# Kernel optimization log

Hardware: AMD Instinct MI355X
Metric: run time of the kernel (lower is better)

Reference implementation:

```python
import jax, jax.numpy as jnp
import numpy as np

HIDDEN = 768
FFN = 3072
E = 8
TOP_K = 2


def setup_inputs() -> dict:
    key = jax.random.key(0)
    k_x, k_r, k_w1, k_w2 = jax.random.split(key, 4)
    x = jax.random.normal(k_x, (1, 1024, HIDDEN), dtype=jnp.float32)
    # nn.Linear(hidden, E, bias=False): weight applied as x @ W^T; store as [H, E]
    bound = 1.0 / np.sqrt(HIDDEN)
    router_w = jax.random.uniform(k_r, (HIDDEN, E), minval=-bound, maxval=bound, dtype=jnp.float32)
    w1 = jax.random.normal(k_w1, (E, HIDDEN, FFN), dtype=jnp.float32) * 0.02
    w2 = jax.random.normal(k_w2, (E, FFN, HIDDEN), dtype=jnp.float32) * 0.02
    return {"x": x, "router_w": router_w, "w1": w1, "w2": w2}


def reference(x, router_w, w1, w2):
    B, T, H = x.shape
    xf = x.reshape(-1, H)                                  # [N, H]
    logits = xf @ router_w                                 # [N, E] (eval mode: no noise)
    probs = jax.nn.softmax(logits, axis=-1)
    top_v, top_i = jax.lax.top_k(probs, TOP_K)             # [N, K]
    top_v = top_v / jnp.sum(top_v, axis=-1, keepdims=True)  # renormalize top-k probs
    # Combine top-k weights into a dense per-expert gate; zero gates make the
    # dense per-expert computation mathematically identical to sparse dispatch.
    gates = jnp.sum(jax.nn.one_hot(top_i, E, dtype=xf.dtype) * top_v[..., None], axis=1)  # [N, E]
    h = jax.nn.gelu(jnp.einsum('nh,ehf->enf', xf, w1), approximate=False)  # [E, N, F]
    y = jnp.einsum('enf,efh->enh', h, w2)                  # [E, N, H]
    out = jnp.einsum('ne,enh->nh', gates, y)               # [N, H]
    return out.reshape(B, T, H)
```

## Files before the change

kernel.cpp:

```cpp
#include <hip/hip_runtime.h>
#include <cmath>

#define NTOK 1024
#define HD   768
#define FF   3072
#define NE   8
#define NSLOT (NTOK * 2)
#define BK   64
#define CLD  130

#define NB_ROUTER 256
#define NB_CONV1  2304
#define NB_CONV2  2304
#define NB_FFN1   3072

typedef unsigned short u16;
typedef unsigned int   u32;
typedef __bf16 bf16x8 __attribute__((ext_vector_type(8)));
typedef float  f32x4  __attribute__((ext_vector_type(4)));
typedef u16    u16x8  __attribute__((ext_vector_type(8)));

__device__ __forceinline__ u16 f2bf(float f) {
  union { float f; u32 u; } v; v.f = f;
  u32 r = v.u + 0x7FFFu + ((v.u >> 16) & 1u);
  return (u16)(r >> 16);
}

__device__ __forceinline__ void load16(const void* g, void* l) {
  __builtin_amdgcn_global_load_lds(
      (const __attribute__((address_space(1))) u32*)g,
      (__attribute__((address_space(3))) u32*)l, 16, 0, 0);
}

__device__ __forceinline__ void conv_tile(
    const float* __restrict__ src, u16* __restrict__ dst,
    int K, int N, int k0, int n0, char* smem, int tid, int lane, int wid)
{
  u16* lt = (u16*)smem;
  const int rr = tid >> 4;
  const int cc = (tid & 15) << 2;

  const float* s0 = src + (size_t)(k0 + rr) * N + n0 + cc;
  float4 v[8];
#pragma unroll
  for (int j = 0; j < 8; ++j) v[j] = *(const float4*)(s0 + (size_t)j * 16 * N);
  __builtin_amdgcn_sched_barrier(0);

#pragma unroll
  for (int j = 0; j < 8; ++j) {
    const int k = j * 16 + rr;
    lt[(cc + 0) * CLD + k] = f2bf(v[j].x); lt[(cc + 1) * CLD + k] = f2bf(v[j].y);
    lt[(cc + 2) * CLD + k] = f2bf(v[j].z); lt[(cc + 3) * CLD + k] = f2bf(v[j].w);
  }
  __syncthreads();

  const int l15 = lane & 15;
  const int r4  = lane >> 4;
#pragma unroll
  for (int s = 0; s < 4; ++s) {
    const int r = wid * 16 + s * 4 + r4;
    u16x8 vv;
#pragma unroll
    for (int d = 0; d < 8; ++d) vv[d] = lt[r * CLD + l15 * 8 + d];
    *(u16x8*)(dst + (size_t)(n0 + r) * K + k0 + l15 * 8) = vv;
  }
}

__global__ __launch_bounds__(256, 4) void conv1_router_kernel(
    const float* __restrict__ w1, u16* __restrict__ w1t,
    const float* __restrict__ x, const float* __restrict__ rw,
    u16* __restrict__ xb, int* __restrict__ counts,
    int* __restrict__ ti, int* __restrict__ tpos, float* __restrict__ tg)
{
  __shared__ __align__(16) char smem[64 * CLD * 2];
  const int tid  = threadIdx.x;
  const int lane = tid & 63;
  const int wid  = tid >> 6;

  if (blockIdx.x >= NB_ROUTER) {
    const int cid = blockIdx.x - NB_ROUTER;
    const int z   = cid / 288;
    const int rem = cid % 288;
    conv_tile(w1 + (size_t)z * HD * FF, w1t + (size_t)z * FF * HD,
              HD, FF, (rem / 48) * 128, (rem % 48) * 64, smem, tid, lane, wid);
  } else {
    const int t = blockIdx.x * 4 + wid;
    const float* xrow = x + (size_t)t * HD;
    u16* xbrow = xb + (size_t)t * HD;

    float acc[NE] = {};
#pragma unroll
    for (int j = 0; j < 12; ++j) {
      const int h = lane + j * 64;
      const float xv = xrow[h];
      xbrow[h] = f2bf(xv);
      const float4 r0 = *(const float4*)(rw + h * 8);
      const float4 r1 = *(const float4*)(rw + h * 8 + 4);
      acc[0] += xv * r0.x; acc[1] += xv * r0.y;
      acc[2] += xv * r0.z; acc[3] += xv * r0.w;
      acc[4] += xv * r1.x; acc[5] += xv * r1.y;
      acc[6] += xv * r1.z; acc[7] += xv * r1.w;
    }
#pragma unroll
    for (int e = 0; e < NE; ++e) {
      float v = acc[e];
#pragma unroll
      for (int off = 32; off; off >>= 1) v += __shfl_down(v, off, 64);
      acc[e] = v;
    }

    if (lane == 0) {
      float v0 = -1e30f, v1 = -1e30f; int i0 = 0, i1 = 0;
#pragma unroll
      for (int e = 0; e < NE; ++e) {
        const float p = acc[e];
        if (p > v0) { v1 = v0; i1 = i0; v0 = p; i0 = e; }
        else if (p > v1) { v1 = p; i1 = e; }
      }
      const float e1 = expf(v1 - v0);
      const float g0 = 1.0f / (1.0f + e1);
      const float g1 = e1 / (1.0f + e1);
      const int p0 = atomicAdd(&counts[i0], 1);
      const int p1 = atomicAdd(&counts[i1], 1);
      ti[2 * t] = i0;  ti[2 * t + 1] = i1;
      tpos[2 * t] = p0; tpos[2 * t + 1] = p1;
      tg[2 * t] = g0;  tg[2 * t + 1] = g1;
    }
  }
}

__global__ __launch_bounds__(1024) void router_scatter(
    const int* __restrict__ counts, const int* __restrict__ ti,
    const int* __restrict__ tpos, const float* __restrict__ tg,
    int* __restrict__ tos, float* __restrict__ gos, int* __restrict__ seg)
{
  __shared__ int offs[NE];
  const int t = threadIdx.x;
  if (t == 0) {
    int o = 0;
    for (int e = 0; e < NE; ++e) {
      offs[e] = o; seg[e] = o; seg[NE + e] = counts[e]; o += counts[e];
    }
  }
  __syncthreads();
  const int i0 = ti[2 * t], i1 = ti[2 * t + 1];
  const int s0 = offs[i0] + tpos[2 * t];
  const int s1 = offs[i1] + tpos[2 * t + 1];
  tos[s0] = t; gos[s0] = tg[2 * t];
  tos[s1] = t; gos[s1] = tg[2 * t + 1];
}

__global__ __launch_bounds__(256) void ffn1_conv2_kernel(
    const u16* __restrict__ xb, const u16* __restrict__ w1t,
    const int* __restrict__ tos, const int* __restrict__ seg,
    u16* __restrict__ hbuf,
    const float* __restrict__ w2, u16* __restrict__ w2t)
{
  __shared__ __align__(16) char smem[25088];
  const int tid  = threadIdx.x;
  const int lane = tid & 63;
  const int wid  = tid >> 6;

  const int g  = blockIdx.x / 7;
  const int r7 = blockIdx.x % 7;

  if (r7 >= 4) {
    const int cid = g * 3 + (r7 - 4);
    const int z   = cid / 288;
    const int rem = cid % 288;
    conv_tile(w2 + (size_t)z * FF * HD, w2t + (size_t)z * HD * FF,
              FF, HD, (rem % 24) * 128, (rem / 24) * 64, smem, tid, lane, wid);
    return;
  }

  const int fid = g * 4 + r7;
  const int e   = fid / 384;
  const int m0  = ((fid / 48) % 8) * 128;
  const int n0  = (fid % 48) * 64;
  const int cnt = seg[NE + e];
  if (m0 >= cnt) return;
  const int start = seg[e];

  u16* As   = (u16*)smem;
  u16* Bs   = (u16*)(smem + 16384);
  int* toks = (int*)(smem + 24576);

  if (tid < 128) toks[tid] = tos[start + min(m0 + tid, cnt - 1)];
  __syncthreads();

  const int rsub = lane >> 3;
  const int c8   = (lane & 7) ^ rsub;

  const u16* ag[4]; u16* al[4];
#pragma unroll
  for (int i = 0; i < 4; ++i) {
    const int rb = wid * 8 + i * 32;
    ag[i] = xb + (size_t)toks[rb + rsub] * HD + c8 * 8;
    al[i] = As + rb * 64;
  }
  const u16* bg[2]; u16* bl[2];
#pragma unroll
  for (int i = 0; i < 2; ++i) {
    const int rb = wid * 8 + i * 32;
    bg[i] = w1t + ((size_t)e * FF + n0 + rb + rsub) * HD + c8 * 8;
    bl[i] = Bs + rb * 64;
  }

  const int wm  = (wid >> 1) << 6;
  const int wn  = (wid & 1) << 5;
  const int q   = lane >> 4;
  const int r16 = lane & 15;

  f32x4 acc[4][2] = {};

  for (int k0 = 0; k0 < HD; k0 += BK) {
#pragma unroll
    for (int i = 0; i < 4; ++i) load16(ag[i] + k0, al[i]);
#pragma unroll
    for (int i = 0; i < 2; ++i) load16(bg[i] + k0, bl[i]);
    __syncthreads();
#pragma unroll
    for (int s = 0; s < 2; ++s) {
      const int pa = ((s << 2) + q) ^ (r16 & 7);
      bf16x8 af[4], bf[2];
#pragma unroll
      for (int t = 0; t < 4; ++t)
        af[t] = *(const bf16x8*)(&As[(wm + t * 16 + r16) * 64 + pa * 8]);
#pragma unroll
      for (int t = 0; t < 2; ++t)
        bf[t] = *(const bf16x8*)(&Bs[(wn + t * 16 + r16) * 64 + pa * 8]);
#pragma unroll
      for (int t = 0; t < 4; ++t)
#pragma unroll
        for (int c = 0; c < 2; ++c)
          acc[t][c] = __builtin_amdgcn_mfma_f32_16x16x32_bf16(af[t], bf[c], acc[t][c], 0, 0, 0);
    }
    __syncthreads();
  }

#pragma unroll
  for (int t = 0; t < 4; ++t) {
    const int mbase = m0 + wm + t * 16 + q * 4;
#pragma unroll
    for (int i = 0; i < 4; ++i) {
      if (mbase + i < cnt) {
        u16* drow = hbuf + (size_t)(start + mbase + i) * FF + n0 + wn;
#pragma unroll
        for (int c = 0; c < 2; ++c) {
          float v = acc[t][c][i];
          v = 0.5f * v * (1.0f + erff(v * 0.70710678118f));
          drow[c * 16 + r16] = f2bf(v);
        }
      }
    }
  }
}

#define KSPLIT 4
#define KSEG   (FF / KSPLIT)

__global__ __launch_bounds__(256) void ffn2_kernel(
    const u16* __restrict__ hbuf, const u16* __restrict__ w2t,
    const int* __restrict__ tos, const float* __restrict__ gos,
    const int* __restrict__ seg, float* __restrict__ out)
{
  const int ez  = blockIdx.z;
  const int e   = ez >> 2;
  const int ks  = ez & 3;
  const int cnt = seg[NE + e];
  const int m0  = blockIdx.y * 128;
  if (m0 >= cnt) return;
  const int start = seg[e];
  const int n0    = blockIdx.x * 64;
  const int kbase = ks * KSEG;

  __shared__ __align__(16) u16 As[128 * 64];
  __shared__ __align__(16) u16 Bs[64 * 64];
  __shared__ int   toks[128];
  __shared__ float gates[128];

  const int tid = threadIdx.x;
  if (tid < 128) {
    const int idx = start + min(m0 + tid, cnt - 1);
    toks[tid]  = tos[idx];
    gates[tid] = gos[idx];
  }
  __syncthreads();

  const int lane = tid & 63;
  const int wid  = tid >> 6;
  const int rsub = lane >> 3;
  const int c8   = (lane & 7) ^ rsub;

  const u16* ag[4]; u16* al[4];
#pragma unroll
  for (int i = 0; i < 4; ++i) {
    const int rb = wid * 8 + i * 32;
    ag[i] = hbuf + (size_t)(start + min(m0 + rb + rsub, cnt - 1)) * FF + kbase + c8 * 8;
    al[i] = As + rb * 64;
  }
  const u16* bg[2]; u16* bl[2];
#pragma unroll
  for (int i = 0; i < 2; ++i) {
    const int rb = wid * 8 + i * 32;
    bg[i] = w2t + ((size_t)e * HD + n0 + rb + rsub) * FF + kbase + c8 * 8;
    bl[i] = Bs + rb * 64;
  }

  const int wm  = (wid >> 1) << 6;
  const int wn  = (wid & 1) << 5;
  const int q   = lane >> 4;
  const int r16 = lane & 15;

  f32x4 acc[4][2] = {};

  for (int k0 = 0; k0 < KSEG; k0 += BK) {
#pragma unroll
    for (int i = 0; i < 4; ++i) load16(ag[i] + k0, al[i]);
#pragma unroll
    for (int i = 0; i < 2; ++i) load16(bg[i] + k0, bl[i]);
    __syncthreads();
#pragma unroll
    for (int s = 0; s < 2; ++s) {
      const int pa = ((s << 2) + q) ^ (r16 & 7);
      bf16x8 af[4], bf[2];
#pragma unroll
      for (int t = 0; t < 4; ++t)
        af[t] = *(const bf16x8*)(&As[(wm + t * 16 + r16) * 64 + pa * 8]);
#pragma unroll
      for (int t = 0; t < 2; ++t)
        bf[t] = *(const bf16x8*)(&Bs[(wn + t * 16 + r16) * 64 + pa * 8]);
#pragma unroll
      for (int t = 0; t < 4; ++t)
#pragma unroll
        for (int c = 0; c < 2; ++c)
          acc[t][c] = __builtin_amdgcn_mfma_f32_16x16x32_bf16(af[t], bf[c], acc[t][c], 0, 0, 0);
    }
    __syncthreads();
  }

#pragma unroll
  for (int t = 0; t < 4; ++t) {
    const int mbase = wm + t * 16 + q * 4;
#pragma unroll
    for (int i = 0; i < 4; ++i) {
      const int mloc = mbase + i;
      if (m0 + mloc < cnt) {
        const int tok  = toks[mloc];
        const float g  = gates[mloc];
        float* drow = out + (size_t)tok * HD + n0 + wn;
#pragma unroll
        for (int c = 0; c < 2; ++c) {
          atomicAdd(drow + c * 16 + r16, g * acc[t][c][i]);
        }
      }
    }
  }
}

extern "C" void kernel_launch(void* const* d_in, const int* in_sizes, int n_in,
                              void* d_out, int out_size, void* d_ws, size_t ws_size,
                              hipStream_t stream) {
  const float* x  = (const float*)d_in[0];
  const float* rw = (const float*)d_in[1];
  const float* w1 = (const float*)d_in[2];
  const float* w2 = (const float*)d_in[3];
  float* out = (float*)d_out;

  char* ws = (char*)d_ws;
  const size_t o_xb    = 0;
  const size_t o_hbuf  = o_xb + (size_t)NTOK * HD * 2;
  const size_t o_tos   = o_hbuf + (size_t)NSLOT * FF * 2;
  const size_t o_gos   = o_tos + (size_t)NSLOT * 4;
  const size_t o_seg   = o_gos + (size_t)NSLOT * 4;
  const size_t o_cnt   = o_seg + 64 * 4;
  const size_t o_ti    = o_cnt + NE * 4;
  const size_t o_tpos  = o_ti + (size_t)NSLOT * 4;
  const size_t o_tg    = o_tpos + (size_t)NSLOT * 4;
  const size_t o_w1t   = (o_tg + (size_t)NSLOT * 4 + 255) & ~(size_t)255;
  const size_t o_w2t   = o_w1t + (size_t)NE * HD * FF * 2;
  u16*   xb    = (u16*)(ws + o_xb);
  u16*   hbuf  = (u16*)(ws + o_hbuf);
  int*   tos   = (int*)(ws + o_tos);
  float* gos   = (float*)(ws + o_gos);
  int*   seg   = (int*)(ws + o_seg);
  int*   cnts  = (int*)(ws + o_cnt);
  int*   ti    = (int*)(ws + o_ti);
  int*   tpos  = (int*)(ws + o_tpos);
  float* tg    = (float*)(ws + o_tg);
  u16*   w1t   = (u16*)(ws + o_w1t);
  u16*   w2t   = (u16*)(ws + o_w2t);

  hipMemsetAsync(d_out, 0, (size_t)NTOK * HD * sizeof(float), stream);
  hipMemsetAsync(cnts, 0, NE * sizeof(int), stream);
  hipLaunchKernelGGL(conv1_router_kernel, dim3(NB_ROUTER + NB_CONV1), dim3(256), 0, stream,
                     w1, w1t, x, rw, xb, cnts, ti, tpos, tg);
  hipLaunchKernelGGL(router_scatter, dim3(1), dim3(1024), 0, stream,
                     cnts, ti, tpos, tg, tos, gos, seg);
  hipLaunchKernelGGL(ffn1_conv2_kernel, dim3((NB_FFN1 + NB_CONV2)), dim3(256), 0, stream,
                     xb, w1t, tos, seg, hbuf, w2, w2t);
  hipLaunchKernelGGL(ffn2_kernel, dim3(HD / 64, NTOK / 128, NE * KSPLIT), dim3(256), 0, stream,
                     hbuf, w2t, tos, gos, seg, out);
}
```

Measured before the change: 273.4 us.

## Fuse router scatter and output zeroing, compact expert tiles, DMA-based weight conversion

The separate scatter kernel and output memset are folded into the router kernel. The last router block, detected with an atomic done counter, builds the per-expert segments, and the router blocks zero the output. The weight fp32-to-bf16 transpose now loads through global_load_lds into a swizzled fp32 LDS tile using 64x64 tiles. FFN1 and FFN2 launch a compacted grid of M-tiles that maps over actual expert counts instead of padding every expert to 1024 tokens, and FFN2 widens its N tile to 128. Together these cut wasted empty blocks and launches, at the cost of more LDS in the conversion tiles and more atomics per FFN2 block.

```diff
diff --git a/kernel.cpp b/kernel.cpp
--- a/kernel.cpp
+++ b/kernel.cpp
@@ -7,12 +7,13 @@
 #define NE   8
 #define NSLOT (NTOK * 2)
 #define BK   64
-#define CLD  130
 
 #define NB_ROUTER 256
-#define NB_CONV1  2304
-#define NB_CONV2  2304
-#define NB_FFN1   3072
+#define NB_CONV   4608
+#define NB_FFN1   1152
+#define KSPLIT    4
+#define KSEG      (FF / KSPLIT)
+#define NB_FFN2   (24 * 6 * KSPLIT)
 
 typedef unsigned short u16;
 typedef unsigned int   u32;
@@ -32,122 +33,146 @@
       (__attribute__((address_space(3))) u32*)l, 16, 0, 0);
 }
 
-__device__ __forceinline__ void conv_tile(
+__device__ __forceinline__ void conv_tile_dma(
     const float* __restrict__ src, u16* __restrict__ dst,
-    int K, int N, int k0, int n0, char* smem, int tid, int lane, int wid)
+    int K, int N, int k0, int n0, float* lt, int tid, int lane, int wid)
 {
-  u16* lt = (u16*)smem;
-  const int rr = tid >> 4;
-  const int cc = (tid & 15) << 2;
-
-  const float* s0 = src + (size_t)(k0 + rr) * N + n0 + cc;
-  float4 v[8];
-#pragma unroll
-  for (int j = 0; j < 8; ++j) v[j] = *(const float4*)(s0 + (size_t)j * 16 * N);
-  __builtin_amdgcn_sched_barrier(0);
-
-#pragma unroll
-  for (int j = 0; j < 8; ++j) {
-    const int k = j * 16 + rr;
-    lt[(cc + 0) * CLD + k] = f2bf(v[j].x); lt[(cc + 1) * CLD + k] = f2bf(v[j].y);
-    lt[(cc + 2) * CLD + k] = f2bf(v[j].z); lt[(cc + 3) * CLD + k] = f2bf(v[j].w);
-  }
-  __syncthreads();
-
-  const int l15 = lane & 15;
-  const int r4  = lane >> 4;
-#pragma unroll
-  for (int s = 0; s < 4; ++s) {
-    const int r = wid * 16 + s * 4 + r4;
+  const int kr = wid * 16;
+#pragma unroll
+  for (int j = 0; j < 4; ++j) {
+    const int k  = kr + j * 4 + (lane >> 4);
+    const int sc = ((lane & 15) * 4) ^ (((k >> 3) & 3) << 3);
+    load16(src + (size_t)(k0 + k) * N + n0 + sc,
+           lt + (size_t)(kr + j * 4) * 64);
+  }
+  __syncthreads();
+#pragma unroll
+  for (int h = 0; h < 2; ++h) {
+    const int c  = tid + h * 256;
+    const int n  = c >> 3;
+    const int ko = c & 7;
+    const int sx = (ko & 3) << 3;
     u16x8 vv;
 #pragma unroll
-    for (int d = 0; d < 8; ++d) vv[d] = lt[r * CLD + l15 * 8 + d];
-    *(u16x8*)(dst + (size_t)(n0 + r) * K + k0 + l15 * 8) = vv;
-  }
-}
-
-__global__ __launch_bounds__(256, 4) void conv1_router_kernel(
+    for (int d = 0; d < 8; ++d)
+      vv[d] = f2bf(lt[(ko * 8 + d) * 64 + (n ^ sx)]);
+    *(u16x8*)(dst + (size_t)(n0 + n) * K + k0 + ko * 8) = vv;
+  }
+}
+
+__global__ __launch_bounds__(256) void conv1_router_kernel(
     const float* __restrict__ w1, u16* __restrict__ w1t,
     const float* __restrict__ x, const float* __restrict__ rw,
-    u16* __restrict__ xb, int* __restrict__ counts,
-    int* __restrict__ ti, int* __restrict__ tpos, float* __restrict__ tg)
+    u16* __restrict__ xb, int* __restrict__ ti, float* __restrict__ tg,
+    int* __restrict__ tos, float* __restrict__ gos, int* __restrict__ seg,
+    int* __restrict__ done, float* __restrict__ out)
 {
-  __shared__ __align__(16) char smem[64 * CLD * 2];
+  __shared__ __align__(16) float lt[64 * 64];
+  __shared__ int soff[NE], scnt[NE], spos[NE], lastFlag;
   const int tid  = threadIdx.x;
   const int lane = tid & 63;
   const int wid  = tid >> 6;
 
   if (blockIdx.x >= NB_ROUTER) {
     const int cid = blockIdx.x - NB_ROUTER;
-    const int z   = cid / 288;
-    const int rem = cid % 288;
-    conv_tile(w1 + (size_t)z * HD * FF, w1t + (size_t)z * FF * HD,
-              HD, FF, (rem / 48) * 128, (rem % 48) * 64, smem, tid, lane, wid);
-  } else {
-    const int t = blockIdx.x * 4 + wid;
-    const float* xrow = x + (size_t)t * HD;
-    u16* xbrow = xb + (size_t)t * HD;
-
-    float acc[NE] = {};
-#pragma unroll
-    for (int j = 0; j < 12; ++j) {
-      const int h = lane + j * 64;
-      const float xv = xrow[h];
-      xbrow[h] = f2bf(xv);
-      const float4 r0 = *(const float4*)(rw + h * 8);
-      const float4 r1 = *(const float4*)(rw + h * 8 + 4);
-      acc[0] += xv * r0.x; acc[1] += xv * r0.y;
-      acc[2] += xv * r0.z; acc[3] += xv * r0.w;
-      acc[4] += xv * r1.x; acc[5] += xv * r1.y;
-      acc[6] += xv * r1.z; acc[7] += xv * r1.w;
-    }
+    const int z   = cid / 576;
+    const int rem = cid % 576;
+    conv_tile_dma(w1 + (size_t)z * HD * FF, w1t + (size_t)z * FF * HD,
+                  HD, FF, (rem / 48) * 64, (rem % 48) * 64, lt, tid, lane, wid);
+    return;
+  }
+
+  {
+    float4* o4 = (float4*)out;
+    const float4 zz = {0.f, 0.f, 0.f, 0.f};
+#pragma unroll
+    for (int i = 0; i < 3; ++i) o4[(size_t)blockIdx.x * 768 + i * 256 + tid] = zz;
+  }
+
+  const int t = blockIdx.x * 4 + wid;
+  const float* xrow = x + (size_t)t * HD;
+  u16* xbrow = xb + (size_t)t * HD;
+
+  float acc[NE] = {};
+#pragma unroll
+  for (int j = 0; j < 12; ++j) {
+    const int h = lane + j * 64;
+    const float xv = xrow[h];
+    xbrow[h] = f2bf(xv);
+    const float4 r0 = *(const float4*)(rw + h * 8);
+    const float4 r1 = *(const float4*)(rw + h * 8 + 4);
+    acc[0] += xv * r0.x; acc[1] += xv * r0.y;
+    acc[2] += xv * r0.z; acc[3] += xv * r0.w;
+    acc[4] += xv * r1.x; acc[5] += xv * r1.y;
+    acc[6] += xv * r1.z; acc[7] += xv * r1.w;
+  }
+#pragma unroll
+  for (int e = 0; e < NE; ++e) {
+    float v = acc[e];
+#pragma unroll
+    for (int off = 32; off; off >>= 1) v += __shfl_down(v, off, 64);
+    acc[e] = v;
+  }
+  if (lane == 0) {
+    float v0 = -1e30f, v1 = -1e30f; int i0 = 0, i1 = 0;
 #pragma unroll
     for (int e = 0; e < NE; ++e) {
-      float v = acc[e];
-#pragma unroll
-      for (int off = 32; off; off >>= 1) v += __shfl_down(v, off, 64);
-      acc[e] = v;
-    }
-
-    if (lane == 0) {
-      float v0 = -1e30f, v1 = -1e30f; int i0 = 0, i1 = 0;
-#pragma unroll
-      for (int e = 0; e < NE; ++e) {
-        const float p = acc[e];
-        if (p > v0) { v1 = v0; i1 = i0; v0 = p; i0 = e; }
-        else if (p > v1) { v1 = p; i1 = e; }
-      }
-      const float e1 = expf(v1 - v0);
-      const float g0 = 1.0f / (1.0f + e1);
-      const float g1 = e1 / (1.0f + e1);
-      const int p0 = atomicAdd(&counts[i0], 1);
-      const int p1 = atomicAdd(&counts[i1], 1);
-      ti[2 * t] = i0;  ti[2 * t + 1] = i1;
-      tpos[2 * t] = p0; tpos[2 * t + 1] = p1;
-      tg[2 * t] = g0;  tg[2 * t + 1] = g1;
-    }
-  }
-}
-
-__global__ __launch_bounds__(1024) void router_scatter(
-    const int* __restrict__ counts, const int* __restrict__ ti,
-    const int* __restrict__ tpos, const float* __restrict__ tg,
-    int* __restrict__ tos, float* __restrict__ gos, int* __restrict__ seg)
-{
-  __shared__ int offs[NE];
-  const int t = threadIdx.x;
-  if (t == 0) {
+      const float p = acc[e];
+      if (p > v0) { v1 = v0; i1 = i0; v0 = p; i0 = e; }
+      else if (p > v1) { v1 = p; i1 = e; }
+    }
+    const float e1 = expf(v1 - v0);
+    ti[2 * t] = i0;      ti[2 * t + 1] = i1;
+    tg[2 * t] = 1.0f / (1.0f + e1);
+    tg[2 * t + 1] = e1 / (1.0f + e1);
+  }
+
+  __syncthreads();
+  __threadfence();
+  if (tid == 0) lastFlag = (atomicAdd(done, 1) == NB_ROUTER - 1);
+  __syncthreads();
+  if (!lastFlag) return;
+  __threadfence();
+
+  if (tid < NE) scnt[tid] = 0;
+  __syncthreads();
+  int   mye[8]; float myg[8];
+#pragma unroll
+  for (int j = 0; j < 8; ++j) {
+    const int s = tid * 8 + j;
+    mye[j] = ti[s]; myg[j] = tg[s];
+    atomicAdd(&scnt[mye[j]], 1);
+  }
+  __syncthreads();
+  if (tid == 0) {
     int o = 0;
     for (int e = 0; e < NE; ++e) {
-      offs[e] = o; seg[e] = o; seg[NE + e] = counts[e]; o += counts[e];
-    }
-  }
-  __syncthreads();
-  const int i0 = ti[2 * t], i1 = ti[2 * t + 1];
-  const int s0 = offs[i0] + tpos[2 * t];
-  const int s1 = offs[i1] + tpos[2 * t + 1];
-  tos[s0] = t; gos[s0] = tg[2 * t];
-  tos[s1] = t; gos[s1] = tg[2 * t + 1];
+      soff[e] = o; seg[e] = o; seg[NE + e] = scnt[e]; o += scnt[e];
+    }
+  }
+  if (tid < NE) spos[tid] = 0;
+  __syncthreads();
+#pragma unroll
+  for (int j = 0; j < 8; ++j) {
+    const int s = tid * 8 + j;
+    const int p = atomicAdd(&spos[mye[j]], 1);
+    const int o = soff[mye[j]] + p;
+    tos[o] = s >> 1;
+    gos[o] = myg[j];
+  }
+}
+
+__device__ __forceinline__ int find_expert(const int* __restrict__ seg,
+                                           int mt, int* m0_out) {
+  int e = -1, m0 = 0, off = 0;
+#pragma unroll
+  for (int ee = 0; ee < NE; ++ee) {
+    const int T = (seg[NE + ee] + 127) >> 7;
+    if (e < 0 && mt < off + T) { e = ee; m0 = (mt - off) << 7; }
+    off += T;
+  }
+  *m0_out = m0;
+  return e;
 }
 
 __global__ __launch_bounds__(256) void ffn1_conv2_kernel(
@@ -161,25 +186,26 @@
   const int lane = tid & 63;
   const int wid  = tid >> 6;
 
-  const int g  = blockIdx.x / 7;
-  const int r7 = blockIdx.x % 7;
-
-  if (r7 >= 4) {
-    const int cid = g * 3 + (r7 - 4);
-    const int z   = cid / 288;
-    const int rem = cid % 288;
-    conv_tile(w2 + (size_t)z * FF * HD, w2t + (size_t)z * HD * FF,
-              FF, HD, (rem % 24) * 128, (rem / 24) * 64, smem, tid, lane, wid);
+  const int g  = blockIdx.x / 5;
+  const int r5 = blockIdx.x % 5;
+
+  if (r5) {
+    const int cid = g * 4 + (r5 - 1);
+    const int z   = cid / 576;
+    const int rem = cid % 576;
+    conv_tile_dma(w2 + (size_t)z * FF * HD, w2t + (size_t)z * HD * FF,
+                  FF, HD, (rem % 48) * 64, (rem / 48) * 64,
+                  (float*)smem, tid, lane, wid);
     return;
   }
 
-  const int fid = g * 4 + r7;
-  const int e   = fid / 384;
-  const int m0  = ((fid / 48) % 8) * 128;
-  const int n0  = (fid % 48) * 64;
-  const int cnt = seg[NE + e];
-  if (m0 >= cnt) return;
+  const int mt = g / 48, nt = g % 48;
+  int m0;
+  const int e = find_expert(seg, mt, &m0);
+  if (e < 0) return;
+  const int cnt   = seg[NE + e];
   const int start = seg[e];
+  const int n0    = nt * 64;
 
   u16* As   = (u16*)smem;
   u16* Bs   = (u16*)(smem + 16384);
@@ -256,26 +282,25 @@
   }
 }
 
-#define KSPLIT 4
-#define KSEG   (FF / KSPLIT)
-
 __global__ __launch_bounds__(256) void ffn2_kernel(
     const u16* __restrict__ hbuf, const u16* __restrict__ w2t,
     const int* __restrict__ tos, const float* __restrict__ gos,
     const int* __restrict__ seg, float* __restrict__ out)
 {
-  const int ez  = blockIdx.z;
-  const int e   = ez >> 2;
-  const int ks  = ez & 3;
-  const int cnt = seg[NE + e];
-  const int m0  = blockIdx.y * 128;
-  if (m0 >= cnt) return;
+  const int fid  = blockIdx.x;
+  const int mt   = fid / 24;
+  const int rest = fid % 24;
+  const int n0   = (rest >> 2) << 7;
+  const int ks   = rest & 3;
+  int m0;
+  const int e = find_expert(seg, mt, &m0);
+  if (e < 0) return;
+  const int cnt   = seg[NE + e];
   const int start = seg[e];
-  const int n0    = blockIdx.x * 64;
   const int kbase = ks * KSEG;
 
   __shared__ __align__(16) u16 As[128 * 64];
-  __shared__ __align__(16) u16 Bs[64 * 64];
+  __shared__ __align__(16) u16 Bs[128 * 64];
   __shared__ int   toks[128];
   __shared__ float gates[128];
 
@@ -299,41 +324,41 @@
     ag[i] = hbuf + (size_t)(start + min(m0 + rb + rsub, cnt - 1)) * FF + kbase + c8 * 8;
     al[i] = As + rb * 64;
   }
-  const u16* bg[2]; u16* bl[2];
-#pragma unroll
-  for (int i = 0; i < 2; ++i) {
+  const u16* bg[4]; u16* bl[4];
+#pragma unroll
+  for (int i = 0; i < 4; ++i) {
     const int rb = wid * 8 + i * 32;
     bg[i] = w2t + ((size_t)e * HD + n0 + rb + rsub) * FF + kbase + c8 * 8;
     bl[i] = Bs + rb * 64;
   }
 
   const int wm  = (wid >> 1) << 6;
-  const int wn  = (wid & 1) << 5;
+  const int wn  = (wid & 1) << 6;
   const int q   = lane >> 4;
   const int r16 = lane & 15;
 
-  f32x4 acc[4][2] = {};
+  f32x4 acc[4][4] = {};
 
   for (int k0 = 0; k0 < KSEG; k0 += BK) {
 #pragma unroll
     for (int i = 0; i < 4; ++i) load16(ag[i] + k0, al[i]);
 #pragma unroll
-    for (int i = 0; i < 2; ++i) load16(bg[i] + k0, bl[i]);
+    for (int i = 0; i < 4; ++i) load16(bg[i] + k0, bl[i]);
     __syncthreads();
 #pragma unroll
     for (int s = 0; s < 2; ++s) {
       const int pa = ((s << 2) + q) ^ (r16 & 7);
-      bf16x8 af[4], bf[2];
+      bf16x8 af[4], bf[4];
 #pragma unroll
       for (int t = 0; t < 4; ++t)
         af[t] = *(const bf16x8*)(&As[(wm + t * 16 + r16) * 64 + pa * 8]);
 #pragma unroll
-      for (int t = 0; t < 2; ++t)
-        bf[t] = *(const bf16x8*)(&Bs[(wn + t * 16 + r16) * 64 + pa * 8]);
+      for (int c = 0; c < 4; ++c)
+        bf[c] = *(const bf16x8*)(&Bs[(wn + c * 16 + r16) * 64 + pa * 8]);
 #pragma unroll
       for (int t = 0; t < 4; ++t)
 #pragma unroll
-        for (int c = 0; c < 2; ++c)
+        for (int c = 0; c < 4; ++c)
           acc[t][c] = __builtin_amdgcn_mfma_f32_16x16x32_bf16(af[t], bf[c], acc[t][c], 0, 0, 0);
     }
     __syncthreads();
@@ -347,12 +372,11 @@
       const int mloc = mbase + i;
       if (m0 + mloc < cnt) {
         const int tok  = toks[mloc];
-        const float g  = gates[mloc];
+        const float gv = gates[mloc];
         float* drow = out + (size_t)tok * HD + n0 + wn;
 #pragma unroll
-        for (int c = 0; c < 2; ++c) {
-          atomicAdd(drow + c * 16 + r16, g * acc[t][c][i]);
-        }
+        for (int c = 0; c < 4; ++c)
+          atomicAdd(drow + c * 16 + r16, gv * acc[t][c][i]);
       }
     }
   }
@@ -373,10 +397,9 @@
   const size_t o_tos   = o_hbuf + (size_t)NSLOT * FF * 2;
   const size_t o_gos   = o_tos + (size_t)NSLOT * 4;
   const size_t o_seg   = o_gos + (size_t)NSLOT * 4;
-  const size_t o_cnt   = o_seg + 64 * 4;
-  const size_t o_ti    = o_cnt + NE * 4;
-  const size_t o_tpos  = o_ti + (size_t)NSLOT * 4;
-  const size_t o_tg    = o_tpos + (size_t)NSLOT * 4;
+  const size_t o_done  = o_seg + 64 * 4;
+  const size_t o_ti    = o_done + 64;
+  const size_t o_tg    = o_ti + (size_t)NSLOT * 4;
   const size_t o_w1t   = (o_tg + (size_t)NSLOT * 4 + 255) & ~(size_t)255;
   const size_t o_w2t   = o_w1t + (size_t)NE * HD * FF * 2;
   u16*   xb    = (u16*)(ws + o_xb);
@@ -384,21 +407,17 @@
   int*   tos   = (int*)(ws + o_tos);
   float* gos   = (float*)(ws + o_gos);
   int*   seg   = (int*)(ws + o_seg);
-  int*   cnts  = (int*)(ws + o_cnt);
+  int*   done  = (int*)(ws + o_done);
   int*   ti    = (int*)(ws + o_ti);
-  int*   tpos  = (int*)(ws + o_tpos);
   float* tg    = (float*)(ws + o_tg);
   u16*   w1t   = (u16*)(ws + o_w1t);
   u16*   w2t   = (u16*)(ws + o_w2t);
 
-  hipMemsetAsync(d_out, 0, (size_t)NTOK * HD * sizeof(float), stream);
-  hipMemsetAsync(cnts, 0, NE * sizeof(int), stream);
-  hipLaunchKernelGGL(conv1_router_kernel, dim3(NB_ROUTER + NB_CONV1), dim3(256), 0, stream,
-                     w1, w1t, x, rw, xb, cnts, ti, tpos, tg);
-  hipLaunchKernelGGL(router_scatter, dim3(1), dim3(1024), 0, stream,
-                     cnts, ti, tpos, tg, tos, gos, seg);
-  hipLaunchKernelGGL(ffn1_conv2_kernel, dim3((NB_FFN1 + NB_CONV2)), dim3(256), 0, stream,
+  hipMemsetAsync(done, 0, 64, stream);
+  hipLaunchKernelGGL(conv1_router_kernel, dim3(NB_ROUTER + NB_CONV), dim3(256), 0, stream,
+                     w1, w1t, x, rw, xb, ti, tg, tos, gos, seg, done, out);
+  hipLaunchKernelGGL(ffn1_conv2_kernel, dim3(NB_FFN1 * 5), dim3(256), 0, stream,
                      xb, w1t, tos, seg, hbuf, w2, w2t);
-  hipLaunchKernelGGL(ffn2_kernel, dim3(HD / 64, NTOK / 128, NE * KSPLIT), dim3(256), 0, stream,
+  hipLaunchKernelGGL(ffn2_kernel, dim3(NB_FFN2), dim3(256), 0, stream,
                      hbuf, w2t, tos, gos, seg, out);
 }
```

After: 273.6 us. About the same (+0.1%).
